# Kernel optimization log

Hardware: AMD Instinct MI355X
Metric: run time of the kernel (lower is better)

## Reference

```python
import jax, jax.numpy as jnp
import numpy as np

B, S, N, D, T = 128, 128, 196, 512, 12


def setup_inputs() -> dict:
    key = jax.random.key(0)
    ks = jax.random.split(key, 20)
    nrm = lambda i, shape, s: jax.random.normal(ks[i], shape, jnp.float32) * s
    w = lambda i, shape: nrm(i, shape, 1.0 / np.sqrt(shape[-1]))
    return {
        "ctx": nrm(0, (B, S, D), 1.0),
        "q": nrm(1, (B, 2 * D), 1.0),
        "k": nrm(2, (B, D, N), 1.0),
        "mem0": nrm(3, (1, D), 0.02),
        "ctrl0": nrm(4, (1, D), 0.02),
        # ControlUnit params
        "Wp": w(5, (T, D, 2 * D)), "bp": jnp.zeros((T, D), jnp.float32),
        "Wcq": w(6, (D, 2 * D)), "bcq": jnp.zeros((D,), jnp.float32),
        "Wca": w(7, (1, D)), "bca": jnp.zeros((1,), jnp.float32),
        # ReadUnit params
        "Wrm": w(8, (D, D)), "brm": jnp.zeros((D,), jnp.float32),
        "Wrc": w(9, (D, 2 * D)), "brc": jnp.zeros((D,), jnp.float32),
        "Wra": w(10, (1, D)), "bra": jnp.zeros((1,), jnp.float32),
        # WriteUnit params
        "Wwc": w(11, (D, 2 * D)), "bwc": jnp.zeros((D,), jnp.float32),
    }


def reference(ctx, q, k, mem0, ctrl0, Wp, bp, Wcq, bcq, Wca, bca,
              Wrm, brm, Wrc, brc, Wra, bra, Wwc, bwc):
    b = q.shape[0]
    c = jnp.broadcast_to(ctrl0, (b, D))
    m = jnp.broadcast_to(mem0, (b, D))
    for t in range(T):
        # --- control unit (alpha_entmax with alpha=1.0 == softmax) ---
        p = q @ Wp[t].T + bp[t]                                # [B, D]
        cc = jnp.concatenate([c, p], axis=1) @ Wcq.T + bcq     # [B, D]
        ctx_p = cc[:, None, :] * ctx                           # [B, S, D]
        aw = jax.nn.softmax(ctx_p @ Wca.T + bca, axis=1)       # [B, S, 1]
        c = (aw * ctx).sum(axis=1)                             # [B, D]
        # --- read unit ---
        mm = (m @ Wrm.T + brm)[:, :, None]                     # [B, D, 1]
        kc = jnp.concatenate([mm * k, k], axis=1)              # [B, 2D, N]
        rc = kc.transpose(0, 2, 1) @ Wrc.T + brc               # [B, N, D]
        logit = ((rc * c[:, None, :]) @ Wra.T + bra)[..., 0]   # [B, N]
        rw = jax.nn.softmax(logit, axis=1)[:, None, :]         # [B, 1, N]
        r = (rw * k).sum(axis=2)                               # [B, D]
        # --- write unit (no self-attention / memory gate) ---
        m = jnp.concatenate([r, m], axis=1) @ Wwc.T + bwc      # [B, D]
    return m
```

## Files before the change

kernel.cpp:

```cpp
#include <hip/hip_runtime.h>
#include <hip/hip_bf16.h>
#include <cstdint>

#define D  512
#define D2 1024
#define BB 128
#define SS 128
#define NN 196
#define TT 12

typedef unsigned short u16;

__device__ __forceinline__ float bf2f(u16 h){
  union { unsigned int u; float f; } v; v.u = ((unsigned int)h) << 16; return v.f;
}

__device__ __forceinline__ float LDX(const void* p, size_t i, int isbf){
  if (isbf) return bf2f(((const u16*)p)[i]);
  return ((const float*)p)[i];
}

__device__ __forceinline__ float4 LD4(const void* p, size_t i, int isbf){
  if (isbf){
    ushort4 w = *(const ushort4*)((const u16*)p + i);
    return make_float4(bf2f(w.x), bf2f(w.y), bf2f(w.z), bf2f(w.w));
  }
  return *(const float4*)((const float*)p + i);
}

__global__ __launch_bounds__(256) void k_detect(const u16* ctx, int* flag){
  __shared__ int cnt;
  if (threadIdx.x == 0) cnt = 0;
  __syncthreads();
  int bad = 0;
  for (int i = threadIdx.x; i < 8192; i += 256){
    int e = (ctx[i] >> 7) & 0xFF;
    if (e == 0xFF || (e != 0 && (e < 90 || e > 160))) bad++;
  }
  atomicAdd(&cnt, bad);
  __syncthreads();
  if (threadIdx.x == 0) *flag = (cnt > 100) ? 0 : 1;
}

__global__ __launch_bounds__(256) void k_prep1(const void* q, const void* Wcq, const void* Wca,
      const void* Wwc, const void* Wrm, const void* Wrc, const void* Wra,
      const void* bp, const void* bcq,
      float* qT, float* W1f, float* Wwcf, float* WrmTf, float* W2f,
      float* P, float* pp2, const int* flag){
  const int isbf = *flag;
  __shared__ float lds[32][33];
  int bk = blockIdx.x, tid = threadIdx.x;
  int tx = tid & 31, ty = tid >> 5;
  if (bk >= 1280){
    int l = bk - 1280;
    for (int idx = l*256 + tid; idx < 786432; idx += 64*256){
      int j = (idx >> 7) & 511;
      pp2[idx] = LDX(bcq, j, isbf) * LDX(Wca, j, isbf);
    }
    return;
  }
  if (bk >= 1216){
    int l = bk - 1216;
    for (int idx = l*256 + tid; idx < 786432; idx += 64*256)
      P[idx] = LDX(bp, idx >> 7, isbf);
    return;
  }
  if (bk >= 1152){
    int l = bk - 1152;
    if (isbf){
      const u16* w = (const u16*)Wrc; const u16* s = (const u16*)Wra;
      for (int idx = l*256 + tid; idx < 524288; idx += 64*256)
        W2f[idx] = bf2f(w[idx]) * bf2f(s[idx >> 10]);
    } else {
      const float* w = (const float*)Wrc; const float* s = (const float*)Wra;
      for (int idx = l*256 + tid; idx < 524288; idx += 64*256)
        W2f[idx] = w[idx] * s[idx >> 10];
    }
    return;
  }
  const void* in = nullptr; const void* scale = nullptr; float* out = nullptr;
  int ld = 0, R = 0, tR = 0, tC = 0;
  if (bk < 128)      { in = q;   ld = 1024; R = 128; out = qT;    tR = bk & 3;  tC = bk >> 2; }
  else if (bk < 384) { int l = bk - 128; in = Wcq; ld = 1024; R = 512; out = W1f;  scale = Wca; tR = l & 15; tC = l >> 4; }
  else if (bk < 896) { int l = bk - 384; in = Wwc; ld = 1024; R = 512; out = Wwcf; tR = l & 15; tC = l >> 4; }
  else               { int l = bk - 896; in = Wrm; ld = 512;  R = 512; out = WrmTf;tR = l & 15; tC = l >> 4; }
  int r0 = tR*32, c0 = tC*32;
  #pragma unroll
  for (int kk = 0; kk < 4; kk++){
    int r = r0 + ty + kk*8;
    float v = LDX(in, (size_t)r*ld + c0 + tx, isbf);
    if (scale) v *= LDX(scale, r, isbf);
    lds[tx][ty + kk*8] = v;
  }
  __syncthreads();
  #pragma unroll
  for (int kk = 0; kk < 4; kk++){
    int oc = ty + kk*8;
    out[(size_t)(c0 + oc)*R + r0 + tx] = lds[oc][tx];
  }
}

__global__ __launch_bounds__(512) void k_P(const float* qT, const void* Wp,
                                           float* P, const int* flag){
  const int isbf = *flag;
  int bk = blockIdx.x;
  int t = bk >> 7; int r = bk & 127; int et = r >> 2; int kc = r & 3;
  int tid = threadIdx.x;
  int b = tid & 127;
  int ih = __builtin_amdgcn_readfirstlane(tid >> 7);
  int e0 = et*16 + ih*4;
  float acc[4] = {0.f, 0.f, 0.f, 0.f};
  size_t wo = (size_t)(t*D + e0)*D2;
  int x0 = kc*256;
  if (isbf){
    const u16* wb = (const u16*)Wp + wo;
    for (int x = x0; x < x0 + 256; x += 8){
      float a[8];
      #pragma unroll
      for (int u = 0; u < 8; u++) a[u] = qT[(x+u)*BB + b];
      #pragma unroll
      for (int kk = 0; kk < 4; kk++){
        ushort4 w0 = *(const ushort4*)(wb + kk*D2 + x);
        ushort4 w1 = *(const ushort4*)(wb + kk*D2 + x + 4);
        acc[kk] += a[0]*bf2f(w0.x) + a[1]*bf2f(w0.y) + a[2]*bf2f(w0.z) + a[3]*bf2f(w0.w)
                 + a[4]*bf2f(w1.x) + a[5]*bf2f(w1.y) + a[6]*bf2f(w1.z) + a[7]*bf2f(w1.w);
      }
    }
  } else {
    const float* wb = (const float*)Wp + wo;
    for (int x = x0; x < x0 + 256; x += 8){
      float a[8];
      #pragma unroll
      for (int u = 0; u < 8; u++) a[u] = qT[(x+u)*BB + b];
      #pragma unroll
      for (int kk = 0; kk < 4; kk++){
        float4 w0 = *(const float4*)(wb + kk*D2 + x);
        float4 w1 = *(const float4*)(wb + kk*D2 + x + 4);
        acc[kk] += a[0]*w0.x + a[1]*w0.y + a[2]*w0.z + a[3]*w0.w
                 + a[4]*w1.x + a[5]*w1.y + a[6]*w1.z + a[7]*w1.w;
      }
    }
  }
  #pragma unroll
  for (int kk = 0; kk < 4; kk++)
    atomicAdd(&P[(size_t)(t*D + e0 + kk)*BB + b], acc[kk]);
}

__global__ __launch_bounds__(512) void k_pp2(const float* P, const void* Wcq,
                                             const void* Wca, float* pp2, const int* flag){
  const int isbf = *flag;
  int bk = blockIdx.x;
  int t = bk >> 6; int r = bk & 63; int jt = r >> 1; int kc = r & 1;
  int tid = threadIdx.x;
  int b = tid & 127;
  int ih = __builtin_amdgcn_readfirstlane(tid >> 7);
  int j0 = jt*16 + ih*4;
  float acc[4] = {0.f, 0.f, 0.f, 0.f};
  int e0k = kc*256;
  if (isbf){
    const u16* w = (const u16*)Wcq;
    for (int e = e0k; e < e0k + 256; e += 8){
      float a[8];
      #pragma unroll
      for (int u = 0; u < 8; u++) a[u] = P[(size_t)(t*D + e + u)*BB + b];
      #pragma unroll
      for (int kk = 0; kk < 4; kk++){
        ushort4 w0 = *(const ushort4*)(w + (size_t)(j0+kk)*D2 + D + e);
        ushort4 w1 = *(const ushort4*)(w + (size_t)(j0+kk)*D2 + D + e + 4);
        acc[kk] += a[0]*bf2f(w0.x) + a[1]*bf2f(w0.y) + a[2]*bf2f(w0.z) + a[3]*bf2f(w0.w)
                 + a[4]*bf2f(w1.x) + a[5]*bf2f(w1.y) + a[6]*bf2f(w1.z) + a[7]*bf2f(w1.w);
      }
    }
  } else {
    const float* w = (const float*)Wcq;
    for (int e = e0k; e < e0k + 256; e += 8){
      float a[8];
      #pragma unroll
      for (int u = 0; u < 8; u++) a[u] = P[(size_t)(t*D + e + u)*BB + b];
      #pragma unroll
      for (int kk = 0; kk < 4; kk++){
        float4 w0 = *(const float4*)(w + (size_t)(j0+kk)*D2 + D + e);
        float4 w1 = *(const float4*)(w + (size_t)(j0+kk)*D2 + D + e + 4);
        acc[kk] += a[0]*w0.x + a[1]*w0.y + a[2]*w0.z + a[3]*w0.w
                 + a[4]*w1.x + a[5]*w1.y + a[6]*w1.z + a[7]*w1.w;
      }
    }
  }
  #pragma unroll
  for (int kk = 0; kk < 4; kk++)
    atomicAdd(&pp2[(size_t)(t*D + j0 + kk)*BB + b], acc[kk] * LDX(Wca, j0 + kk, isbf));
}

__global__ __launch_bounds__(256) void k_initA(const void* ctrl0, const void* mem0,
                                               const void* Wcq, const void* Wca,
                                               const void* Wrm, const void* brm,
                                               float* ubase, float* mmb, const int* flag){
  const int isbf = *flag;
  int bk = blockIdx.x, tid = threadIdx.x;
  int lane = tid & 63, w = tid >> 6;
  int grp = lane >> 3, k = lane & 7;
  int isU = (bk < 16);
  int o = (isU ? bk : bk - 16)*32 + w*8 + grp;
  const void* vec = isU ? ctrl0 : mem0;
  const void* mat = isU ? Wcq : Wrm;
  int ld = isU ? D2 : D;
  float acc = 0.f;
  #pragma unroll 4
  for (int it = 0; it < 16; it++){
    int d = it*32 + k*4;
    float4 v = LD4(vec, d, isbf);
    float4 m = LD4(mat, (size_t)o*ld + d, isbf);
    acc += v.x*m.x + v.y*m.y + v.z*m.z + v.w*m.w;
  }
  acc += __shfl_xor(acc, 1, 64);
  acc += __shfl_xor(acc, 2, 64);
  acc += __shfl_xor(acc, 4, 64);
  if (k == 0){
    if (isU) ubase[o] = acc * LDX(Wca, o, isbf);
    else     mmb[o]   = acc + LDX(brm, o, isbf);
  }
}

__global__ __launch_bounds__(256) void k_initB(const float* ubase, const float* mmb,
                                               const void* mem0, const float* pp2,
                                               float* u0, float* mm0, float* act0,
                                               const int* flag){
  const int isbf = *flag;
  for (int idx = blockIdx.x*256 + threadIdx.x; idx < 3*D*BB; idx += 96*256){
    if (idx < D*BB)            u0[idx] = ubase[idx >> 7] + pp2[idx];
    else if (idx < 2*D*BB)   { int x = idx - D*BB;   mm0[x] = mmb[x >> 7]; }
    else                     { int x = idx - 2*D*BB; act0[D*BB + x] = LDX(mem0, x >> 7, isbf); }
  }
}

__device__ void attn1_body(const void* ctx, const float* u_cur, float* cbuf,
                           int b, int tid, int isbf, float* sm){
  float* cch = sm;
  float* lg  = sm + 8192;
  int lane = tid & 63, wv = tid >> 6;
  float ur[8];
  #pragma unroll
  for (int kk = 0; kk < 4; kk++){
    ur[kk]   = u_cur[(lane*4 + kk)*BB + b];
    ur[4+kk] = u_cur[(256 + lane*4 + kk)*BB + b];
  }
  float mv = -INFINITY, ls = 0.f, o = 0.f;
  for (int c = 0; c < 8; c++){
    int s0 = c*16;
    #pragma unroll
    for (int rr = 0; rr < 2; rr++){
      int loc = rr*8 + wv;
      int s = s0 + loc;
      float4 c0, c1;
      if (isbf){
        const u16* crow = (const u16*)ctx + ((size_t)(b*SS + s))*D;
        ushort4 h0 = *(const ushort4*)(crow + lane*4);
        ushort4 h1 = *(const ushort4*)(crow + 256 + lane*4);
        c0 = make_float4(bf2f(h0.x), bf2f(h0.y), bf2f(h0.z), bf2f(h0.w));
        c1 = make_float4(bf2f(h1.x), bf2f(h1.y), bf2f(h1.z), bf2f(h1.w));
      } else {
        const float* crow = (const float*)ctx + ((size_t)(b*SS + s))*D;
        c0 = *(const float4*)(crow + lane*4);
        c1 = *(const float4*)(crow + 256 + lane*4);
      }
      *(float4*)&cch[loc*512 + lane*4]       = c0;
      *(float4*)&cch[loc*512 + 256 + lane*4] = c1;
      float dot = ur[0]*c0.x + ur[1]*c0.y + ur[2]*c0.z + ur[3]*c0.w
                + ur[4]*c1.x + ur[5]*c1.y + ur[6]*c1.z + ur[7]*c1.w;
      #pragma unroll
      for (int off = 32; off; off >>= 1) dot += __shfl_down(dot, off, 64);
      if (lane == 0) lg[loc] = dot;
    }
    __syncthreads();
    float Mc = lg[0];
    #pragma unroll
    for (int s = 1; s < 16; s++) Mc = fmaxf(Mc, lg[s]);
    float mn = fmaxf(mv, Mc);
    float sc = __expf(mv - mn);
    ls *= sc; o *= sc;
    #pragma unroll
    for (int s = 0; s < 16; s++){
      float e = __expf(lg[s] - mn);
      ls += e;
      o += e * cch[s*512 + tid];
    }
    mv = mn;
    __syncthreads();
  }
  cbuf[tid*BB + b] = o / ls;
}

__device__ void attn2_body(const void* kmat, const float* wbuf, const float* mm_cur,
                           float* act_cur, int b, int tid, int isbf, float* sm){
  float* u2 = sm;
  float* lg = sm + 512;
  float* red= sm + 768;
  float* ps = sm + 1024;
  u2[tid] = wbuf[tid*BB + b]*mm_cur[tid*BB + b] + wbuf[(D + tid)*BB + b];
  __syncthreads();
  {
    int half = tid >> 8;
    int n = tid & 255;
    float part = 0.f;
    if (n < NN){
      float c[8];
      #pragma unroll
      for (int u = 0; u < 8; u++) c[u] = 0.f;
      int d0 = half*256;
      if (isbf){
        const u16* kb = (const u16*)kmat + (size_t)b*D*NN + n;
        for (int dd = 0; dd < 256; dd += 8){
          #pragma unroll
          for (int u = 0; u < 8; u++) c[u] += u2[d0+dd+u]*bf2f(kb[(size_t)(d0+dd+u)*NN]);
        }
      } else {
        const float* kb = (const float*)kmat + (size_t)b*D*NN + n;
        for (int dd = 0; dd < 256; dd += 8){
          #pragma unroll
          for (int u = 0; u < 8; u++) c[u] += u2[d0+dd+u]*kb[(size_t)(d0+dd+u)*NN];
        }
      }
      part = (((c[0]+c[1]) + (c[2]+c[3])) + ((c[4]+c[5]) + (c[6]+c[7])));
    }
    ps[half*256 + n] = part;
  }
  __syncthreads();
  if (tid < 256){
    float logit = (tid < NN) ? (ps[tid] + ps[256 + tid]) : -INFINITY;
    lg[tid] = logit; red[tid] = logit;
  }
  __syncthreads();
  for (int off = 128; off; off >>= 1){ if (tid < off) red[tid] = fmaxf(red[tid], red[tid+off]); __syncthreads(); }
  float M = red[0];
  __syncthreads();
  if (tid < 256){ float e = (tid < NN) ? __expf(lg[tid] - M) : 0.f; lg[tid] = e; red[tid] = e; }
  __syncthreads();
  for (int off = 128; off; off >>= 1){ if (tid < off) red[tid] += red[tid+off]; __syncthreads(); }
  float inv = 1.f / red[0];
  int lane = tid & 63, wv = tid >> 6;
  for (int i = 0; i < 32; i++){
    int dA = wv + i*16, dB = dA + 8;
    float p, qv;
    if (isbf){
      const u16* krA = (const u16*)kmat + (size_t)b*D*NN + (size_t)dA*NN;
      const u16* krB = (const u16*)kmat + (size_t)b*D*NN + (size_t)dB*NN;
      p  = lg[lane]*bf2f(krA[lane]) + lg[lane+64]*bf2f(krA[lane+64]) + lg[lane+128]*bf2f(krA[lane+128]);
      qv = lg[lane]*bf2f(krB[lane]) + lg[lane+64]*bf2f(krB[lane+64]) + lg[lane+128]*bf2f(krB[lane+128]);
      if (lane < NN - 192){
        p  += lg[lane+192]*bf2f(krA[lane+192]);
        qv += lg[lane+192]*bf2f(krB[lane+192]);
      }
    } else {
      const float* krA = (const float*)kmat + (size_t)b*D*NN + (size_t)dA*NN;
      const float* krB = (const float*)kmat + (size_t)b*D*NN + (size_t)dB*NN;
      p  = lg[lane]*krA[lane] + lg[lane+64]*krA[lane+64] + lg[lane+128]*krA[lane+128];
      qv = lg[lane]*krB[lane] + lg[lane+64]*krB[lane+64] + lg[lane+128]*krB[lane+128];
      if (lane < NN - 192){
        p  += lg[lane+192]*krA[lane+192];
        qv += lg[lane+192]*krB[lane+192];
      }
    }
    #pragma unroll
    for (int off = 32; off; off >>= 1){
      p  += __shfl_down(p , off, 64);
      qv += __shfl_down(qv, off, 64);
    }
    if (lane == 0){
      act_cur[dA*BB + b] = p  * inv;
      act_cur[dB*BB + b] = qv * inv;
    }
  }
}

__global__ __launch_bounds__(512) void k_KA(const void* ctx, const float* u_cur, float* cbuf,
                                            const float* act_prev, float* act_cur,
                                            float* wbuf, float* mmbuf, float* u_nxt,
                                            const float* pp2_next, const void* brm,
                                            const float* Wwcf, int t, const int* flag){
  __shared__ float sm[8208];
  int bk = blockIdx.x, tid = threadIdx.x;
  const int isbf = *flag;
  if (bk < 128){
    attn1_body(ctx, u_cur, cbuf, bk, tid, isbf, sm);
    return;
  }
  int b = tid & 127;
  int ih = __builtin_amdgcn_readfirstlane(tid >> 7);
  if (bk < 640){
    if (t == 0) return;
    int l = bk - 128;
    int it = l >> 3, kc = l & 7;
    int ih0 = ih & 1, ih1 = ih >> 1;
    int i0 = it*8 + ih0*4;
    int e0 = kc*128 + ih1*64;
    float acc[4] = {0.f,0.f,0.f,0.f};
    for (int e = e0; e < e0 + 64; e += 8){
      float av[8];
      #pragma unroll
      for (int u = 0; u < 8; u++) av[u] = act_prev[(size_t)(e+u)*BB + b];
      #pragma unroll
      for (int u = 0; u < 8; u++){
        float4 w0 = *(const float4*)(Wwcf + (size_t)(e+u)*D + i0);
        acc[0]+=av[u]*w0.x; acc[1]+=av[u]*w0.y; acc[2]+=av[u]*w0.z; acc[3]+=av[u]*w0.w;
      }
    }
    #pragma unroll
    for (int kk = 0; kk < 4; kk++)
      atomicAdd(&act_cur[(size_t)(D + i0 + kk)*BB + b], acc[kk]);
  } else if (bk < 704){
    int l = bk - 640;
    for (int x = l*512 + tid; x < D2*BB; x += 64*512) wbuf[x] = 0.f;
  } else if (bk < 736){
    if (t == 0) return;
    int l = bk - 704;
    for (int x = l*512 + tid; x < D*BB; x += 32*512) mmbuf[x] = LDX(brm, x >> 7, isbf);
  } else {
    if (t >= TT-1) return;
    int l = bk - 736;
    for (int x = l*512 + tid; x < D*BB; x += 32*512) u_nxt[x] = pp2_next[x];
  }
}

__global__ __launch_bounds__(256) void k_KB(const float* cbuf, const float* W2f, float* wbuf,
                                            const float* act_cur, const float* WrmTf,
                                            float* mmbuf, int t){
  int bk = blockIdx.x, tid = threadIdx.x;
  int b = tid & 127;
  int ih = __builtin_amdgcn_readfirstlane(tid >> 7);
  if (bk < 512){
    int et = bk >> 2, kc = bk & 3;
    int e0 = et*8 + ih*4;
    float acc[4] = {0.f, 0.f, 0.f, 0.f};
    int j0 = kc*128;
    for (int j = j0; j < j0 + 128; j += 8){
      float av[8];
      #pragma unroll
      for (int u = 0; u < 8; u++) av[u] = cbuf[(j+u)*BB + b];
      #pragma unroll
      for (int u = 0; u < 8; u++){
        float4 wv = *(const float4*)(W2f + (size_t)(j+u)*D2 + e0);
        acc[0] += av[u]*wv.x; acc[1] += av[u]*wv.y;
        acc[2] += av[u]*wv.z; acc[3] += av[u]*wv.w;
      }
    }
    #pragma unroll
    for (int kk = 0; kk < 4; kk++) atomicAdd(&wbuf[(e0+kk)*BB + b], acc[kk]);
  } else {
    if (t == 0) return;
    int l = bk - 512;
    int it = l >> 2, kc = l & 3;
    int i0 = it*8 + ih*4;
    float acc[4] = {0.f, 0.f, 0.f, 0.f};
    int d0 = kc*128;
    for (int d = d0; d < d0 + 128; d += 8){
      float av[8];
      #pragma unroll
      for (int u = 0; u < 8; u++) av[u] = act_cur[(size_t)(D + d + u)*BB + b];
      #pragma unroll
      for (int u = 0; u < 8; u++){
        float4 wv = *(const float4*)(WrmTf + (size_t)(d+u)*D + i0);
        acc[0] += av[u]*wv.x; acc[1] += av[u]*wv.y;
        acc[2] += av[u]*wv.z; acc[3] += av[u]*wv.w;
      }
    }
    #pragma unroll
    for (int kk = 0; kk < 4; kk++) atomicAdd(&mmbuf[(i0+kk)*BB + b], acc[kk]);
  }
}

__global__ __launch_bounds__(512) void k_KC(const void* kmat, const float* wbuf,
                                            const float* mmbuf, float* act_cur,
                                            const float* cbuf, const float* W1f, float* u_nxt,
                                            float* act_nxt, const void* bwc,
                                            int t, const int* flag){
  __shared__ float sm[1536];
  int bk = blockIdx.x, tid = threadIdx.x;
  const int isbf = *flag;
  if (bk < 128){
    attn2_body(kmat, wbuf, mmbuf, act_cur, bk, tid, isbf, sm);
    return;
  }
  int b = tid & 127;
  int ih = __builtin_amdgcn_readfirstlane(tid >> 7);
  if (bk < 384){
    if (t >= TT-1) return;
    int l = bk - 128;
    int jt = l >> 1, kc = l & 1;
    int j = jt*4 + ih;
    float c0 = 0.f, c1 = 0.f, c2 = 0.f, c3 = 0.f, c4 = 0.f, c5 = 0.f, c6 = 0.f, c7 = 0.f;
    int e0 = kc*256;
    for (int e = e0; e < e0 + 256; e += 8){
      c0 += cbuf[(e  )*BB + b] * W1f[(size_t)(e  )*D + j];
      c1 += cbuf[(e+1)*BB + b] * W1f[(size_t)(e+1)*D + j];
      c2 += cbuf[(e+2)*BB + b] * W1f[(size_t)(e+2)*D + j];
      c3 += cbuf[(e+3)*BB + b] * W1f[(size_t)(e+3)*D + j];
      c4 += cbuf[(e+4)*BB + b] * W1f[(size_t)(e+4)*D + j];
      c5 += cbuf[(e+5)*BB + b] * W1f[(size_t)(e+5)*D + j];
      c6 += cbuf[(e+6)*BB + b] * W1f[(size_t)(e+6)*D + j];
      c7 += cbuf[(e+7)*BB + b] * W1f[(size_t)(e+7)*D + j];
    }
    float acc = (((c0+c1)+(c2+c3)) + ((c4+c5)+(c6+c7)));
    atomicAdd(&u_nxt[(size_t)j*BB + b], acc);
  } else {
    if (t >= TT-1) return;
    int l = bk - 384;
    for (int x = l*512 + tid; x < D*BB; x += 32*512)
      act_nxt[D*BB + x] = LDX(bwc, x >> 7, isbf);
  }
}

__global__ __launch_bounds__(512) void k_mout(const float* act_fin, const float* Wwcf,
                                              const void* bwc, void* out, const int* flag){
  const int isbf = *flag;
  int bk = blockIdx.x, tid = threadIdx.x;
  int b = tid & 127;
  int ih = __builtin_amdgcn_readfirstlane(tid >> 7);
  int i = bk*4 + ih;
  float c0 = 0.f, c1 = 0.f, c2 = 0.f, c3 = 0.f, c4 = 0.f, c5 = 0.f, c6 = 0.f, c7 = 0.f;
  for (int e = 0; e < D2; e += 8){
    c0 += act_fin[(size_t)(e  )*BB + b] * Wwcf[(size_t)(e  )*D + i];
    c1 += act_fin[(size_t)(e+1)*BB + b] * Wwcf[(size_t)(e+1)*D + i];
    c2 += act_fin[(size_t)(e+2)*BB + b] * Wwcf[(size_t)(e+2)*D + i];
    c3 += act_fin[(size_t)(e+3)*BB + b] * Wwcf[(size_t)(e+3)*D + i];
    c4 += act_fin[(size_t)(e+4)*BB + b] * Wwcf[(size_t)(e+4)*D + i];
    c5 += act_fin[(size_t)(e+5)*BB + b] * Wwcf[(size_t)(e+5)*D + i];
    c6 += act_fin[(size_t)(e+6)*BB + b] * Wwcf[(size_t)(e+6)*D + i];
    c7 += act_fin[(size_t)(e+7)*BB + b] * Wwcf[(size_t)(e+7)*D + i];
  }
  float acc = LDX(bwc, i, isbf) + (((c0+c1)+(c2+c3)) + ((c4+c5)+(c6+c7)));
  if (isbf) ((__hip_bfloat16*)out)[(size_t)b*D + i] = __float2bfloat16(acc);
  else      ((float*)out)[(size_t)b*D + i] = acc;
}

extern "C" void kernel_launch(void* const* d_in, const int* in_sizes, int n_in,
                              void* d_out, int out_size, void* d_ws, size_t ws_size,
                              hipStream_t stream){
  const void* ctx  = d_in[0];
  const void* q    = d_in[1];
  const void* kmat = d_in[2];
  const void* mem0 = d_in[3];
  const void* ctrl0= d_in[4];
  const void* Wp   = d_in[5];
  const void* bp   = d_in[6];
  const void* Wcq  = d_in[7];
  const void* bcq  = d_in[8];
  const void* Wca  = d_in[9];
  const void* Wrm  = d_in[11];
  const void* brm  = d_in[12];
  const void* Wrc  = d_in[13];
  const void* Wra  = d_in[15];
  const void* Wwc  = d_in[17];
  const void* bwc  = d_in[18];

  float* W      = (float*)d_ws;
  float* qT     = W;
  float* P      = W + 131072;
  float* pp2    = W + 917504;
  float* W1f    = W + 1703936;
  float* W2f    = W + 1966080;
  float* Wwcf   = W + 2490368;
  float* WrmTf  = W + 3014656;
  float* cbuf   = W + 3276800;
  float* wbuf   = W + 3342336;
  float* mmbuf  = W + 3473408;
  float* actb   = W + 3538944;
  float* ubuf   = W + 3801088;
  int*   flag   = (int*)(W + 3932160);
  float* ubase  = W + 3932224;
  float* mmb    = W + 3932736;

  hipLaunchKernelGGL(k_detect, dim3(1), dim3(256), 0, stream, (const u16*)ctx, flag);
  hipLaunchKernelGGL(k_prep1, dim3(1344), dim3(256), 0, stream,
                     q, Wcq, Wca, Wwc, Wrm, Wrc, Wra, bp, bcq,
                     qT, W1f, Wwcf, WrmTf, W2f, P, pp2, flag);
  hipLaunchKernelGGL(k_P,    dim3(1536), dim3(512), 0, stream, qT, Wp, P, flag);
  hipLaunchKernelGGL(k_pp2,  dim3(768), dim3(512), 0, stream, P, Wcq, Wca, pp2, flag);
  hipLaunchKernelGGL(k_initA, dim3(32), dim3(256), 0, stream,
                     ctrl0, mem0, Wcq, Wca, Wrm, brm, ubase, mmb, flag);
  hipLaunchKernelGGL(k_initB, dim3(96), dim3(256), 0, stream,
                     ubase, mmb, mem0, pp2, ubuf, mmbuf, actb, flag);

  for (int t = 0; t < TT; t++){
    int cur = t & 1, nxt = 1 - cur;
    float* act_cur = actb + cur*131072;
    float* act_prev = actb + nxt*131072;
    hipLaunchKernelGGL(k_KA, dim3(768), dim3(512), 0, stream,
                       ctx, ubuf + cur*65536, cbuf,
                       act_prev, act_cur, wbuf, mmbuf, ubuf + nxt*65536,
                       pp2 + ((t+1 < TT) ? (t+1)*65536 : 0), brm, Wwcf, t, flag);
    hipLaunchKernelGGL(k_KB, dim3(768), dim3(256), 0, stream,
                       cbuf, W2f, wbuf, act_cur, WrmTf, mmbuf, t);
    hipLaunchKernelGGL(k_KC, dim3(416), dim3(512), 0, stream,
                       kmat, wbuf, mmbuf, act_cur,
                       cbuf, W1f, ubuf + nxt*65536,
                       act_prev, bwc, t, flag);
  }
  hipLaunchKernelGGL(k_mout, dim3(128), dim3(512), 0, stream,
                     actb + 131072, Wwcf, bwc, d_out, flag);
}
```

Baseline: 1.225 ms.

## Fold init kernel into prep, unroll P GEMV, split final projection with atomics

Merges the k_initA blocks into k_prep1, which removes one launch. The k_P inner loop is unrolled to 16 elements for more loads in flight. The final write projection is split across 512 blocks that atomically accumulate into a bias-preinitialized buffer, and a separate transpose kernel writes the output. This raises parallelism in the tail GEMV at the cost of atomics and an extra launch; KC now also initializes the bias on the final step.

```diff
diff --git a/kernel.cpp b/kernel.cpp
--- a/kernel.cpp
+++ b/kernel.cpp
@@ -44,13 +44,39 @@
 
 __global__ __launch_bounds__(256) void k_prep1(const void* q, const void* Wcq, const void* Wca,
       const void* Wwc, const void* Wrm, const void* Wrc, const void* Wra,
-      const void* bp, const void* bcq,
+      const void* bp, const void* bcq, const void* ctrl0, const void* mem0, const void* brm,
       float* qT, float* W1f, float* Wwcf, float* WrmTf, float* W2f,
-      float* P, float* pp2, const int* flag){
+      float* P, float* pp2, float* ubase, float* mmb, const int* flag){
   const int isbf = *flag;
   __shared__ float lds[32][33];
   int bk = blockIdx.x, tid = threadIdx.x;
   int tx = tid & 31, ty = tid >> 5;
+  if (bk >= 1344){
+    int ib = bk - 1344;
+    int lane = tid & 63, w = tid >> 6;
+    int grp = lane >> 3, k = lane & 7;
+    int isU = (ib < 16);
+    int o = (isU ? ib : ib - 16)*32 + w*8 + grp;
+    const void* vec = isU ? ctrl0 : mem0;
+    const void* mat = isU ? Wcq : Wrm;
+    int ld = isU ? D2 : D;
+    float acc = 0.f;
+    #pragma unroll 4
+    for (int it = 0; it < 16; it++){
+      int d = it*32 + k*4;
+      float4 v = LD4(vec, d, isbf);
+      float4 m = LD4(mat, (size_t)o*ld + d, isbf);
+      acc += v.x*m.x + v.y*m.y + v.z*m.z + v.w*m.w;
+    }
+    acc += __shfl_xor(acc, 1, 64);
+    acc += __shfl_xor(acc, 2, 64);
+    acc += __shfl_xor(acc, 4, 64);
+    if (k == 0){
+      if (isU) ubase[o] = acc * LDX(Wca, o, isbf);
+      else     mmb[o]   = acc + LDX(brm, o, isbf);
+    }
+    return;
+  }
   if (bk >= 1280){
     int l = bk - 1280;
     for (int idx = l*256 + tid; idx < 786432; idx += 64*256){
@@ -114,30 +140,38 @@
   int x0 = kc*256;
   if (isbf){
     const u16* wb = (const u16*)Wp + wo;
-    for (int x = x0; x < x0 + 256; x += 8){
-      float a[8];
-      #pragma unroll
-      for (int u = 0; u < 8; u++) a[u] = qT[(x+u)*BB + b];
+    for (int x = x0; x < x0 + 256; x += 16){
+      float a[16];
+      #pragma unroll
+      for (int u = 0; u < 16; u++) a[u] = qT[(x+u)*BB + b];
       #pragma unroll
       for (int kk = 0; kk < 4; kk++){
         ushort4 w0 = *(const ushort4*)(wb + kk*D2 + x);
         ushort4 w1 = *(const ushort4*)(wb + kk*D2 + x + 4);
+        ushort4 w2 = *(const ushort4*)(wb + kk*D2 + x + 8);
+        ushort4 w3 = *(const ushort4*)(wb + kk*D2 + x + 12);
         acc[kk] += a[0]*bf2f(w0.x) + a[1]*bf2f(w0.y) + a[2]*bf2f(w0.z) + a[3]*bf2f(w0.w)
-                 + a[4]*bf2f(w1.x) + a[5]*bf2f(w1.y) + a[6]*bf2f(w1.z) + a[7]*bf2f(w1.w);
+                 + a[4]*bf2f(w1.x) + a[5]*bf2f(w1.y) + a[6]*bf2f(w1.z) + a[7]*bf2f(w1.w)
+                 + a[8]*bf2f(w2.x) + a[9]*bf2f(w2.y) + a[10]*bf2f(w2.z) + a[11]*bf2f(w2.w)
+                 + a[12]*bf2f(w3.x) + a[13]*bf2f(w3.y) + a[14]*bf2f(w3.z) + a[15]*bf2f(w3.w);
       }
     }
   } else {
     const float* wb = (const float*)Wp + wo;
-    for (int x = x0; x < x0 + 256; x += 8){
-      float a[8];
-      #pragma unroll
-      for (int u = 0; u < 8; u++) a[u] = qT[(x+u)*BB + b];
+    for (int x = x0; x < x0 + 256; x += 16){
+      float a[16];
+      #pragma unroll
+      for (int u = 0; u < 16; u++) a[u] = qT[(x+u)*BB + b];
       #pragma unroll
       for (int kk = 0; kk < 4; kk++){
         float4 w0 = *(const float4*)(wb + kk*D2 + x);
         float4 w1 = *(const float4*)(wb + kk*D2 + x + 4);
+        float4 w2 = *(const float4*)(wb + kk*D2 + x + 8);
+        float4 w3 = *(const float4*)(wb + kk*D2 + x + 12);
         acc[kk] += a[0]*w0.x + a[1]*w0.y + a[2]*w0.z + a[3]*w0.w
-                 + a[4]*w1.x + a[5]*w1.y + a[6]*w1.z + a[7]*w1.w;
+                 + a[4]*w1.x + a[5]*w1.y + a[6]*w1.z + a[7]*w1.w
+                 + a[8]*w2.x + a[9]*w2.y + a[10]*w2.z + a[11]*w2.w
+                 + a[12]*w3.x + a[13]*w3.y + a[14]*w3.z + a[15]*w3.w;
       }
     }
   }
@@ -189,36 +223,6 @@
   #pragma unroll
   for (int kk = 0; kk < 4; kk++)
     atomicAdd(&pp2[(size_t)(t*D + j0 + kk)*BB + b], acc[kk] * LDX(Wca, j0 + kk, isbf));
-}
-
-__global__ __launch_bounds__(256) void k_initA(const void* ctrl0, const void* mem0,
-                                               const void* Wcq, const void* Wca,
-                                               const void* Wrm, const void* brm,
-                                               float* ubase, float* mmb, const int* flag){
-  const int isbf = *flag;
-  int bk = blockIdx.x, tid = threadIdx.x;
-  int lane = tid & 63, w = tid >> 6;
-  int grp = lane >> 3, k = lane & 7;
-  int isU = (bk < 16);
-  int o = (isU ? bk : bk - 16)*32 + w*8 + grp;
-  const void* vec = isU ? ctrl0 : mem0;
-  const void* mat = isU ? Wcq : Wrm;
-  int ld = isU ? D2 : D;
-  float acc = 0.f;
-  #pragma unroll 4
-  for (int it = 0; it < 16; it++){
-    int d = it*32 + k*4;
-    float4 v = LD4(vec, d, isbf);
-    float4 m = LD4(mat, (size_t)o*ld + d, isbf);
-    acc += v.x*m.x + v.y*m.y + v.z*m.z + v.w*m.w;
-  }
-  acc += __shfl_xor(acc, 1, 64);
-  acc += __shfl_xor(acc, 2, 64);
-  acc += __shfl_xor(acc, 4, 64);
-  if (k == 0){
-    if (isU) ubase[o] = acc * LDX(Wca, o, isbf);
-    else     mmb[o]   = acc + LDX(brm, o, isbf);
-  }
 }
 
 __global__ __launch_bounds__(256) void k_initB(const float* ubase, const float* mmb,
@@ -502,34 +506,64 @@
     float acc = (((c0+c1)+(c2+c3)) + ((c4+c5)+(c6+c7)));
     atomicAdd(&u_nxt[(size_t)j*BB + b], acc);
   } else {
-    if (t >= TT-1) return;
     int l = bk - 384;
     for (int x = l*512 + tid; x < D*BB; x += 32*512)
       act_nxt[D*BB + x] = LDX(bwc, x >> 7, isbf);
   }
 }
 
-__global__ __launch_bounds__(512) void k_mout(const float* act_fin, const float* Wwcf,
-                                              const void* bwc, void* out, const int* flag){
-  const int isbf = *flag;
+__global__ __launch_bounds__(512) void k_moutA(const float* act_fin, const float* Wwcf,
+                                               float* act_out){
   int bk = blockIdx.x, tid = threadIdx.x;
   int b = tid & 127;
   int ih = __builtin_amdgcn_readfirstlane(tid >> 7);
-  int i = bk*4 + ih;
-  float c0 = 0.f, c1 = 0.f, c2 = 0.f, c3 = 0.f, c4 = 0.f, c5 = 0.f, c6 = 0.f, c7 = 0.f;
-  for (int e = 0; e < D2; e += 8){
-    c0 += act_fin[(size_t)(e  )*BB + b] * Wwcf[(size_t)(e  )*D + i];
-    c1 += act_fin[(size_t)(e+1)*BB + b] * Wwcf[(size_t)(e+1)*D + i];
-    c2 += act_fin[(size_t)(e+2)*BB + b] * Wwcf[(size_t)(e+2)*D + i];
-    c3 += act_fin[(size_t)(e+3)*BB + b] * Wwcf[(size_t)(e+3)*D + i];
-    c4 += act_fin[(size_t)(e+4)*BB + b] * Wwcf[(size_t)(e+4)*D + i];
-    c5 += act_fin[(size_t)(e+5)*BB + b] * Wwcf[(size_t)(e+5)*D + i];
-    c6 += act_fin[(size_t)(e+6)*BB + b] * Wwcf[(size_t)(e+6)*D + i];
-    c7 += act_fin[(size_t)(e+7)*BB + b] * Wwcf[(size_t)(e+7)*D + i];
-  }
-  float acc = LDX(bwc, i, isbf) + (((c0+c1)+(c2+c3)) + ((c4+c5)+(c6+c7)));
-  if (isbf) ((__hip_bfloat16*)out)[(size_t)b*D + i] = __float2bfloat16(acc);
-  else      ((float*)out)[(size_t)b*D + i] = acc;
+  int it = bk >> 3, kc = bk & 7;
+  int ih0 = ih & 1, ih1 = ih >> 1;
+  int i0 = it*8 + ih0*4;
+  int e0 = kc*128 + ih1*64;
+  float acc[4] = {0.f,0.f,0.f,0.f};
+  for (int e = e0; e < e0 + 64; e += 8){
+    float av[8];
+    #pragma unroll
+    for (int u = 0; u < 8; u++) av[u] = act_fin[(size_t)(e+u)*BB + b];
+    #pragma unroll
+    for (int u = 0; u < 8; u++){
+      float4 w0 = *(const float4*)(Wwcf + (size_t)(e+u)*D + i0);
+      acc[0]+=av[u]*w0.x; acc[1]+=av[u]*w0.y; acc[2]+=av[u]*w0.z; acc[3]+=av[u]*w0.w;
+    }
+  }
+  #pragma unroll
+  for (int kk = 0; kk < 4; kk++)
+    atomicAdd(&act_out[(size_t)(D + i0 + kk)*BB + b], acc[kk]);
+}
+
+__global__ __launch_bounds__(256) void k_outT(const float* act_fin, void* out, const int* flag){
+  const int isbf = *flag;
+  __shared__ float lds[32][33];
+  int bk = blockIdx.x;
+  int it = bk >> 2, bt = bk & 3;
+  int tx = threadIdx.x & 31, ty = threadIdx.x >> 5;
+  #pragma unroll
+  for (int kk = 0; kk < 4; kk++){
+    int i = it*32 + ty + kk*8;
+    lds[tx][ty + kk*8] = act_fin[(size_t)(D + i)*BB + bt*32 + tx];
+  }
+  __syncthreads();
+  if (isbf){
+    __hip_bfloat16* o = (__hip_bfloat16*)out;
+    #pragma unroll
+    for (int kk = 0; kk < 4; kk++){
+      int bb = bt*32 + ty + kk*8;
+      o[(size_t)bb*D + it*32 + tx] = __float2bfloat16(lds[ty + kk*8][tx]);
+    }
+  } else {
+    float* o = (float*)out;
+    #pragma unroll
+    for (int kk = 0; kk < 4; kk++){
+      int bb = bt*32 + ty + kk*8;
+      o[(size_t)bb*D + it*32 + tx] = lds[ty + kk*8][tx];
+    }
+  }
 }
 
 extern "C" void kernel_launch(void* const* d_in, const int* in_sizes, int n_in,
@@ -570,13 +604,11 @@
   float* mmb    = W + 3932736;
 
   hipLaunchKernelGGL(k_detect, dim3(1), dim3(256), 0, stream, (const u16*)ctx, flag);
-  hipLaunchKernelGGL(k_prep1, dim3(1344), dim3(256), 0, stream,
-                     q, Wcq, Wca, Wwc, Wrm, Wrc, Wra, bp, bcq,
-                     qT, W1f, Wwcf, WrmTf, W2f, P, pp2, flag);
+  hipLaunchKernelGGL(k_prep1, dim3(1376), dim3(256), 0, stream,
+                     q, Wcq, Wca, Wwc, Wrm, Wrc, Wra, bp, bcq, ctrl0, mem0, brm,
+                     qT, W1f, Wwcf, WrmTf, W2f, P, pp2, ubase, mmb, flag);
   hipLaunchKernelGGL(k_P,    dim3(1536), dim3(512), 0, stream, qT, Wp, P, flag);
   hipLaunchKernelGGL(k_pp2,  dim3(768), dim3(512), 0, stream, P, Wcq, Wca, pp2, flag);
-  hipLaunchKernelGGL(k_initA, dim3(32), dim3(256), 0, stream,
-                     ctrl0, mem0, Wcq, Wca, Wrm, brm, ubase, mmb, flag);
   hipLaunchKernelGGL(k_initB, dim3(96), dim3(256), 0, stream,
                      ubase, mmb, mem0, pp2, ubuf, mmbuf, actb, flag);
 
@@ -593,8 +625,9 @@
     hipLaunchKernelGGL(k_KC, dim3(416), dim3(512), 0, stream,
                        kmat, wbuf, mmbuf, act_cur,
                        cbuf, W1f, ubuf + nxt*65536,
-                       act_prev, bwc, t, flag);
-  }
-  hipLaunchKernelGGL(k_mout, dim3(128), dim3(512), 0, stream,
-                     actb + 131072, Wwcf, bwc, d_out, flag);
-}
+                       actb + nxt*131072, bwc, t, flag);
+  }
+  hipLaunchKernelGGL(k_moutA, dim3(512), dim3(512), 0, stream,
+                     actb + 131072, Wwcf, actb);
+  hipLaunchKernelGGL(k_outT, dim3(64), dim3(256), 0, stream, actb, d_out, flag);
+}
```

After: 1.109 ms. 1.1x faster.
